# Optimization experiments

Measured on AMD Instinct MI355X. Metric: run time of the kernel, lower is better.

## Reference

```python
import jax, jax.numpy as jnp
import numpy as np

EPS = 1e-6
NUM_HEADS = 8
GAMMA = 0.999


def simple_rms_norm(x):
    # SimpleRMSNorm: x / ||x|| * sqrt(d) == x / sqrt(mean(x^2))
    return x * jax.lax.rsqrt(jnp.mean(x * x, axis=-1, keepdims=True) + EPS)


def setup_inputs() -> dict:
    key = jax.random.key(0)
    ks = jax.random.split(key, 12)
    B, N, M, E = 64, 14, 14, 512
    D1 = 2 * E              # expand_ratio * embed_dim = 1024
    RPE = 512               # rpe_embedding
    s = 0.02
    inp = {
        "x": jax.random.normal(ks[0], (B, N, M, E), jnp.float32),
        "H": N,
        "W": M,
        "Wu": jax.random.normal(ks[1], (E, D1), jnp.float32) * s,
        "bu": jnp.zeros((D1,), jnp.float32),
        "Wv": jax.random.normal(ks[2], (E, D1), jnp.float32) * s,
        "bv": jnp.zeros((D1,), jnp.float32),
        "Wo": jax.random.normal(ks[3], (D1, E), jnp.float32) * s,
        "bo": jnp.zeros((E,), jnp.float32),
        "rpe_pos_w": jax.random.normal(ks[4], (2, RPE), jnp.float32) * s,
        "rpe_pos_b": jnp.zeros((RPE,), jnp.float32),
        "rpe_w1": jax.random.normal(ks[5], (RPE, RPE), jnp.float32) * s,
        "rpe_b1": jnp.zeros((RPE,), jnp.float32),
        "rpe_w2": jax.random.normal(ks[6], (RPE, RPE), jnp.float32) * s,
        "rpe_b2": jnp.zeros((RPE,), jnp.float32),
        "rpe_w3": jax.random.normal(ks[7], (RPE, RPE), jnp.float32) * s,
        "rpe_b3": jnp.zeros((RPE,), jnp.float32),
        "rpe_out_w": jax.random.normal(ks[8], (RPE, D1), jnp.float32) * s,
        "rpe_out_b": jnp.zeros((D1,), jnp.float32),
    }
    return inp


def gtu2d_forward(x, Wu, bu, Wv, bv, Wo, bo,
                  rpe_pos_w, rpe_pos_b, rpe_w1, rpe_b1, rpe_w2, rpe_b2,
                  rpe_w3, rpe_b3, rpe_out_w, rpe_out_b):
    B, n, m, E = x.shape
    d1 = Wu.shape[1]
    hd = d1 // NUM_HEADS
    # dual gated projections
    u = jax.nn.silu(x @ Wu + bu)                      # (B, n, m, d1)
    v = jax.nn.silu(x @ Wv + bv)
    v = v.reshape(B, n, m, NUM_HEADS, hd).transpose(0, 3, 1, 2, 4)  # (B, h, n, m, d)

    # --- Tno2D: RPE MLP produces Toeplitz coefficients for relative positions ---
    ii = jnp.arange(-(n - 1), n, dtype=jnp.float32)
    jj = jnp.arange(-(m - 1), m, dtype=jnp.float32)
    pos = jnp.stack(jnp.meshgrid(ii, jj, indexing="ij"), axis=-1)  # (2n-1, 2m-1, 2)
    r = pos @ rpe_pos_w + rpe_pos_b
    for w, b in ((rpe_w1, rpe_b1), (rpe_w2, rpe_b2), (rpe_w3, rpe_b3)):
        r = jax.nn.relu(simple_rms_norm(r)) @ w + b
    r = jax.nn.relu(simple_rms_norm(r)) @ rpe_out_w + rpe_out_b  # (2n-1, 2m-1, h*d)
    a = r.reshape(2 * n - 1, 2 * m - 1, NUM_HEADS, hd).transpose(2, 0, 1, 3)
    # decay: gamma^(|i|+|j|)
    dist = jnp.abs(pos[..., 0]) + jnp.abs(pos[..., 1])  # (2n-1, 2m-1)
    a = a * (GAMMA ** dist)[None, :, :, None]

    # embed coefficients into circular kernel (h, 2n, 2m, d); index n / m are zero
    t = jnp.zeros((NUM_HEADS, 2 * n, 2 * m, hd), a.dtype)
    t = t.at[:, :n, :m].set(a[:, n - 1:, m - 1:])
    t = t.at[:, n + 1:, :m].set(a[:, :n - 1, m - 1:])
    t = t.at[:, :n, m + 1:].set(a[:, n - 1:, :m - 1])
    t = t.at[:, n + 1:, m + 1:].set(a[:, :n - 1, :m - 1])

    # 2D Toeplitz matvec via circular convolution / FFT
    xf = jnp.fft.rfft2(v, s=(2 * n, 2 * m), axes=(2, 3))
    tf = jnp.fft.rfft2(t, s=(2 * n, 2 * m), axes=(1, 2))
    y = jnp.fft.irfft2(xf * tf[None], s=(2 * n, 2 * m), axes=(2, 3))[:, :, :n, :m, :]
    y = y.transpose(0, 2, 3, 1, 4).reshape(B, n, m, d1)  # 'b h n m d -> b n m (h d)'

    return (u * y) @ Wo + bo


def reference(x, H, W, Wu, bu, Wv, bv, Wo, bo,
              rpe_pos_w, rpe_pos_b, rpe_w1, rpe_b1, rpe_w2, rpe_b2,
              rpe_w3, rpe_b3, rpe_out_w, rpe_out_b):
    # H, W are unused by Gtu2d.forward (spatial dims are carried by x)
    return gtu2d_forward(x, Wu, bu, Wv, bv, Wo, bo,
                         rpe_pos_w, rpe_pos_b, rpe_w1, rpe_b1, rpe_w2, rpe_b2,
                         rpe_w3, rpe_b3, rpe_out_w, rpe_out_b)
```

## Files before the change

### kernel.cpp

```cpp
#include <hip/hip_runtime.h>
#include <hip/hip_bf16.h>

typedef __hip_bfloat16 bf16;
typedef __attribute__((ext_vector_type(8))) short bf16x8;
typedef __attribute__((ext_vector_type(4))) float f32x4;

constexpr int NB    = 64;
constexpr int EE    = 512;
constexpr int RPOS  = 27 * 27;
constexpr int ROWS  = NB * 14 * 14;

#define RMS_EPS 1e-6f
#define GAMMA_LOG2 (-0.00144344319f)

__device__ __forceinline__ void  stf(float* p, float v) { *p = v; }
__device__ __forceinline__ void  stf(bf16* p, float v)  { *p = __float2bfloat16(v); }

__device__ __forceinline__ void gload_lds16(const bf16* g, bf16* l) {
    __builtin_amdgcn_global_load_lds(
        (const __attribute__((address_space(1))) void*)g,
        (__attribute__((address_space(3))) void*)l, 16, 0, 0);
}

#define VMCNT(n) asm volatile("s_waitcnt vmcnt(" #n ")" ::: "memory")

__global__ __launch_bounds__(256) void k_prep(const float* __restrict__ Wu,
                                              const float* __restrict__ Wv,
                                              const float* __restrict__ Wo,
                                              const float* __restrict__ w1,
                                              const float* __restrict__ w2,
                                              const float* __restrict__ w3,
                                              const float* __restrict__ wOut,
                                              const float* __restrict__ bu,
                                              const float* __restrict__ bv,
                                              const float* __restrict__ x,
                                              bf16* __restrict__ WuvT,
                                              bf16* __restrict__ WoT,
                                              bf16* __restrict__ w1T,
                                              bf16* __restrict__ w2T,
                                              bf16* __restrict__ w3T,
                                              bf16* __restrict__ wOutT,
                                              float* __restrict__ biasUv,
                                              bf16* __restrict__ xb) {
    __shared__ float t[32][33];
    const int tid = threadIdx.x;
    int b = blockIdx.x;

    const float* src = nullptr; bf16* dst = nullptr; int R = 0, C = 0, nbx = 0;
    if (b < 512)        { src = Wu;   dst = WuvT;                      R = 512;  C = 1024; nbx = 32; }
    else if (b < 1024)  { b -= 512;   src = Wv; dst = WuvT + (size_t)1024 * 512; R = 512; C = 1024; nbx = 32; }
    else if (b < 1536)  { b -= 1024;  src = Wo;   dst = WoT;           R = 1024; C = 512;  nbx = 16; }
    else if (b < 1792)  { b -= 1536;  src = w1;   dst = w1T;           R = 512;  C = 512;  nbx = 16; }
    else if (b < 2048)  { b -= 1792;  src = w2;   dst = w2T;           R = 512;  C = 512;  nbx = 16; }
    else if (b < 2304)  { b -= 2048;  src = w3;   dst = w3T;           R = 512;  C = 512;  nbx = 16; }
    else if (b < 2816)  { b -= 2304;  src = wOut; dst = wOutT;         R = 512;  C = 1024; nbx = 32; }
    else if (b < 2824) {
        int c = (b - 2816) * 256 + tid;
        if (c < 2048) biasUv[c] = (c < 1024) ? bu[c] : bv[c - 1024];
        return;
    } else {
        int i = (b - 2824) * 256 + tid;
        float4 v = *(const float4*)&x[(size_t)i * 4];
        bf16* d = &xb[(size_t)i * 4];
        d[0] = __float2bfloat16(v.x);
        d[1] = __float2bfloat16(v.y);
        d[2] = __float2bfloat16(v.z);
        d[3] = __float2bfloat16(v.w);
        return;
    }
    int bx = (b % nbx) * 32;
    int by = (b / nbx) * 32;
    int tx = tid & 31, ty = tid >> 5;
    #pragma unroll
    for (int i = 0; i < 4; ++i)
        t[ty + i * 8][tx] = src[(size_t)(by + ty + i * 8) * C + bx + tx];
    __syncthreads();
    #pragma unroll
    for (int i = 0; i < 4; ++i)
        dst[(size_t)(bx + ty + i * 8) * R + by + tx] = __float2bfloat16(t[tx][ty + i * 8]);
}

__global__ void k_rpe_pos_norm(const float* __restrict__ w, const float* __restrict__ bias,
                               bf16* __restrict__ out) {
    int p = blockIdx.x;
    float ii = (float)(p / 27 - 13);
    float jj = (float)(p % 27 - 13);
    int c0 = threadIdx.x, c1 = threadIdx.x + 256;
    float v0 = ii * w[c0] + jj * w[512 + c0] + bias[c0];
    float v1 = ii * w[c1] + jj * w[512 + c1] + bias[c1];
    float s = v0 * v0 + v1 * v1;
    #pragma unroll
    for (int off = 32; off; off >>= 1) s += __shfl_down(s, off, 64);
    __shared__ float ps[4];
    if ((threadIdx.x & 63) == 0) ps[threadIdx.x >> 6] = s;
    __syncthreads();
    float tot = ps[0] + ps[1] + ps[2] + ps[3];
    float scale = rsqrtf(tot * (1.0f / 512.0f) + RMS_EPS);
    out[(size_t)p * 512 + c0] = __float2bfloat16(fmaxf(v0 * scale, 0.0f));
    out[(size_t)p * 512 + c1] = __float2bfloat16(fmaxf(v1 * scale, 0.0f));
}

template <typename TO>
__global__ void k_rmsnorm_relu(const float* __restrict__ in, TO* __restrict__ out) {
    int r = blockIdx.x;
    const float* x = in + (size_t)r * 512;
    float v0 = x[threadIdx.x];
    float v1 = x[threadIdx.x + 256];
    float s = v0 * v0 + v1 * v1;
    #pragma unroll
    for (int off = 32; off; off >>= 1) s += __shfl_down(s, off, 64);
    __shared__ float ps[4];
    if ((threadIdx.x & 63) == 0) ps[threadIdx.x >> 6] = s;
    __syncthreads();
    float tot = ps[0] + ps[1] + ps[2] + ps[3];
    float scale = rsqrtf(tot * (1.0f / 512.0f) + RMS_EPS);
    stf(&out[(size_t)r * 512 + threadIdx.x],       fmaxf(v0 * scale, 0.0f));
    stf(&out[(size_t)r * 512 + threadIdx.x + 256], fmaxf(v1 * scale, 0.0f));
}

template <int EPI, typename TO>
__global__ __launch_bounds__(256) void k_mgemm_s(const bf16* __restrict__ A,
                                                 const bf16* __restrict__ Bt,
                                                 const float* __restrict__ bias,
                                                 TO* __restrict__ out,
                                                 int M, int N, int K) {
    __shared__ bf16 As[64 * 32];
    __shared__ bf16 Bs[64 * 32];
    const int tid = threadIdx.x;
    const int m0 = blockIdx.y * 64;
    const int n0 = blockIdx.x * 64;
    const int lane = tid & 63;
    const int w = tid >> 6;
    const int lr = lane & 15;
    const int lk = (lane >> 4) * 8;

    f32x4 acc[4] = {};
    const int row = tid >> 2;
    const int seg = (tid & 3) * 8;

    for (int k0 = 0; k0 < K; k0 += 32) {
        gload_lds16(&A[(size_t)(m0 + row) * K + k0 + seg], &As[tid * 8]);
        gload_lds16(&Bt[(size_t)(n0 + row) * K + k0 + seg], &Bs[tid * 8]);
        __syncthreads();
        bf16x8 af = *(const bf16x8*)&As[(w * 16 + lr) * 32 + lk];
        #pragma unroll
        for (int j = 0; j < 4; ++j) {
            bf16x8 bf = *(const bf16x8*)&Bs[(j * 16 + lr) * 32 + lk];
            acc[j] = __builtin_amdgcn_mfma_f32_16x16x32_bf16(af, bf, acc[j], 0, 0, 0);
        }
        __syncthreads();
    }

    const int crow = (lane >> 4) * 4;
    const int ccol = lane & 15;
    #pragma unroll
    for (int j = 0; j < 4; ++j) {
        int gc = n0 + j * 16 + ccol;
        float bb = bias[gc];
        #pragma unroll
        for (int r = 0; r < 4; ++r) {
            int gr = m0 + w * 16 + crow + r;
            if (gr < M) {
                float val = acc[j][r] + bb;
                if (EPI == 2) {
                    int i = gr / 27, jj = gr % 27;
                    val *= exp2f((float)(abs(i - 13) + abs(jj - 13)) * GAMMA_LOG2);
                }
                stf(&out[(size_t)gr * N + gc], val);
            }
        }
    }
}

template <int EPI, typename TO>
__global__ __launch_bounds__(256) void k_mgemm(const bf16* __restrict__ A, int lda,
                                               const bf16* __restrict__ Bt,
                                               const float* __restrict__ bias,
                                               TO* __restrict__ out, int ldo,
                                               int M, int N, int K) {
    __shared__ bf16 As[128 * 32];
    __shared__ bf16 Bs[128 * 32];
    const int tid = threadIdx.x;
    const int m0 = blockIdx.y * 128;
    const int n0 = blockIdx.x * 128;
    const int lane = tid & 63;
    const int w = tid >> 6;
    const int wr = (w >> 1) * 64;
    const int wc = (w & 1) * 64;
    const int lr = lane & 15;
    const int lk = (lane >> 4) * 8;

    f32x4 acc[4][4] = {};

    for (int k0 = 0; k0 < K; k0 += 32) {
        #pragma unroll
        for (int t = 0; t < 2; ++t) {
            int flat = t * 256 + tid;
            int row = flat >> 2;
            int seg = (flat & 3) * 8;
            gload_lds16(&A[(size_t)(m0 + row) * lda + k0 + seg], &As[flat * 8]);
            gload_lds16(&Bt[(size_t)(n0 + row) * K + k0 + seg], &Bs[flat * 8]);
        }
        __syncthreads();
        bf16x8 af[4], bf[4];
        #pragma unroll
        for (int i = 0; i < 4; ++i) {
            af[i] = *(const bf16x8*)&As[(wr + i * 16 + lr) * 32 + lk];
            bf[i] = *(const bf16x8*)&Bs[(wc + i * 16 + lr) * 32 + lk];
        }
        #pragma unroll
        for (int i = 0; i < 4; ++i)
            #pragma unroll
            for (int j = 0; j < 4; ++j)
                acc[i][j] = __builtin_amdgcn_mfma_f32_16x16x32_bf16(af[i], bf[j], acc[i][j], 0, 0, 0);
        __syncthreads();
    }

    const int crow = (lane >> 4) * 4;
    const int ccol = lane & 15;
    #pragma unroll
    for (int i = 0; i < 4; ++i)
        #pragma unroll
        for (int j = 0; j < 4; ++j) {
            int gc = n0 + wc + j * 16 + ccol;
            float bb = bias[gc];
            #pragma unroll
            for (int r = 0; r < 4; ++r) {
                int gr = m0 + wr + i * 16 + crow + r;
                float val = acc[i][j][r] + bb;
                if (EPI == 1) val = val / (1.0f + expf(-val));
                stf(&out[(size_t)gr * ldo + gc], val);
            }
        }
}

template <int KT, int EPI, typename TO>
__global__ __launch_bounds__(512, 2) void k_mgemm8(const bf16* __restrict__ A, int lda,
                                                   const bf16* __restrict__ Bt,
                                                   const float* __restrict__ bias,
                                                   TO* __restrict__ out, int ldo,
                                                   int nb ) {
    constexpr int K = KT * 64;
    __shared__ __align__(16) char lds[131072];

    const int tid = threadIdx.x;
    const int lane = tid & 63;
    const int wid = tid >> 6;
    const int wr = wid >> 2;
    const int wc = wid & 3;

    int wgid = blockIdx.x;
    if ((gridDim.x & 7) == 0) {
        int cpx = gridDim.x >> 3;
        wgid = (wgid & 7) * cpx + (wgid >> 3);
    }
    const int m0 = (wgid / nb) * 256;
    const int n0 = (wgid % nb) * 256;

    auto ldsA = [&](int d, int kh) -> char* { return (char*)lds + d * 32768 + kh * 16384; };
    auto ldsB = [&](int d, int kh) -> char* { return (char*)lds + 65536 + d * 32768 + kh * 16384; };

    auto stage = [&](int op, int kh, int tt) {
        char* base = op ? ldsB(tt & 1, kh) : ldsA(tt & 1, kh);
        const bf16* g = op ? Bt : A;
        const int rowbase = op ? n0 : m0;
        const int ldr = op ? K : lda;
        #pragma unroll
        for (int l = 0; l < 2; ++l) {
            int q = tid + l * 512;
            int r = q >> 2;
            int cl = (q & 3) ^ ((r ^ (r >> 2)) & 3);
            const bf16* src = g + (size_t)(rowbase + r) * ldr + tt * 64 + kh * 32 + cl * 8;
            gload_lds16(src, (bf16*)(base + q * 16));
        }
    };
    auto rdA = [&](int d, int ks, int mi) -> bf16x8 {
        int row = wr * 128 + mi * 16 + (lane & 15);
        int ch = (lane >> 4) ^ ((row ^ (row >> 2)) & 3);
        return *(const bf16x8*)(ldsA(d, ks) + row * 64 + ch * 16);
    };
    auto rdB = [&](int d, int ks, int nj) -> bf16x8 {
        int row = wc * 64 + nj * 16 + (lane & 15);
        int ch = (lane >> 4) ^ ((row ^ (row >> 2)) & 3);
        return *(const bf16x8*)(ldsB(d, ks) + row * 64 + ch * 16);
    };

    f32x4 acc[8][4] = {};
    bf16x8 aF[4], bF[4];

    stage(0, 0, 0); stage(1, 0, 0); stage(0, 1, 0); stage(1, 1, 0);
    stage(0, 0, 1); stage(1, 0, 1);
    VMCNT(8);
    __builtin_amdgcn_s_barrier();
    __builtin_amdgcn_sched_barrier(0);

    #pragma unroll
    for (int t = 0; t < KT; ++t) {
        const int d = t & 1;
        #pragma unroll
        for (int mi = 0; mi < 4; ++mi) aF[mi] = rdA(d, 0, mi);
        #pragma unroll
        for (int nj = 0; nj < 4; ++nj) bF[nj] = rdB(d, 0, nj);
        if (t + 1 < KT) stage(0, 1, t + 1);
        __builtin_amdgcn_s_barrier();
        __builtin_amdgcn_s_setprio(1);
        #pragma unroll
        for (int mi = 0; mi < 4; ++mi)
            #pragma unroll
            for (int nj = 0; nj < 4; ++nj)
                acc[mi][nj] = __builtin_amdgcn_mfma_f32_16x16x32_bf16(aF[mi], bF[nj], acc[mi][nj], 0, 0, 0);
        __builtin_amdgcn_s_setprio(0);
        __builtin_amdgcn_s_barrier();
        #pragma unroll
        for (int mi = 0; mi < 4; ++mi) aF[mi] = rdA(d, 0, mi + 4);
        if (t + 1 < KT) stage(1, 1, t + 1);
        if (t + 1 < KT) { VMCNT(8); } else { VMCNT(0); }
        __builtin_amdgcn_s_barrier();
        __builtin_amdgcn_sched_barrier(0);
        __builtin_amdgcn_s_setprio(1);
        #pragma unroll
        for (int mi = 0; mi < 4; ++mi)
            #pragma unroll
            for (int nj = 0; nj < 4; ++nj)
                acc[mi + 4][nj] = __builtin_amdgcn_mfma_f32_16x16x32_bf16(aF[mi], bF[nj], acc[mi + 4][nj], 0, 0, 0);
        __builtin_amdgcn_s_setprio(0);
        __builtin_amdgcn_s_barrier();
        #pragma unroll
        for (int mi = 0; mi < 4; ++mi) aF[mi] = rdA(d, 1, mi);
        #pragma unroll
        for (int nj = 0; nj < 4; ++nj) bF[nj] = rdB(d, 1, nj);
        if (t + 2 < KT) stage(0, 0, t + 2);
        __builtin_amdgcn_s_barrier();
        __builtin_amdgcn_s_setprio(1);
        #pragma unroll
        for (int mi = 0; mi < 4; ++mi)
            #pragma unroll
            for (int nj = 0; nj < 4; ++nj)
                acc[mi][nj] = __builtin_amdgcn_mfma_f32_16x16x32_bf16(aF[mi], bF[nj], acc[mi][nj], 0, 0, 0);
        __builtin_amdgcn_s_setprio(0);
        __builtin_amdgcn_s_barrier();
        #pragma unroll
        for (int mi = 0; mi < 4; ++mi) aF[mi] = rdA(d, 1, mi + 4);
        if (t + 2 < KT) stage(1, 0, t + 2);
        if (t + 2 < KT)      { VMCNT(8); }
        else if (t + 1 < KT) { VMCNT(4); }
        __builtin_amdgcn_s_barrier();
        __builtin_amdgcn_sched_barrier(0);
        __builtin_amdgcn_s_setprio(1);
        #pragma unroll
        for (int mi = 0; mi < 4; ++mi)
            #pragma unroll
            for (int nj = 0; nj < 4; ++nj)
                acc[mi + 4][nj] = __builtin_amdgcn_mfma_f32_16x16x32_bf16(aF[mi], bF[nj], acc[mi + 4][nj], 0, 0, 0);
        __builtin_amdgcn_s_setprio(0);
        __builtin_amdgcn_s_barrier();
    }

    const int crow = (lane >> 4) * 4;
    const int ccol = lane & 15;
    #pragma unroll
    for (int mi = 0; mi < 8; ++mi)
        #pragma unroll
        for (int nj = 0; nj < 4; ++nj) {
            int gc = n0 + wc * 64 + nj * 16 + ccol;
            float bb = bias[gc];
            #pragma unroll
            for (int r = 0; r < 4; ++r) {
                int gr = m0 + wr * 128 + mi * 16 + crow + r;
                float val = acc[mi][nj][r] + bb;
                if (EPI == 1) val = val / (1.0f + expf(-val));
                stf(&out[(size_t)gr * ldo + gc], val);
            }
        }
}

__global__ __launch_bounds__(256) void k_vt(const bf16* __restrict__ uv,
                                            bf16* __restrict__ Vt) {
    const int c0 = blockIdx.x * 64;
    const int b  = blockIdx.y;
    const int tid = threadIdx.x;
    __shared__ bf16 t[196][66];
    for (int f = tid; f < 196 * 64; f += 256) {
        int ij = f >> 6, cl = f & 63;
        t[ij][cl] = uv[((size_t)b * 196 + ij) * 2048 + 1024 + c0 + cl];
    }
    __syncthreads();
    const bf16 z = __float2bfloat16(0.0f);
    for (int f = tid; f < 64 * 224; f += 256) {
        int cl = f / 224, ij = f - cl * 224;
        Vt[((size_t)(c0 + cl) * 64 + b) * 224 + ij] = (ij < 196) ? t[ij][cl] : z;
    }
}

__global__ __launch_bounds__(256) void k_convm(const bf16* __restrict__ Ab,
                                               const bf16* __restrict__ Vt,
                                               bf16* __restrict__ Yt, int cbase) {
    __shared__ __align__(16) bf16 Ts[112 * 232];
    __shared__ bf16 As[736];
    const int mh = blockIdx.x;
    const int cl = blockIdx.y;
    const int c = cbase + cl;
    const int tid = threadIdx.x;
    const int mbase = mh * 112;

    for (int e = tid; e < 729; e += 256)
        As[e] = Ab[(size_t)e * 1024 + c];
    __syncthreads();

    const bf16 z = __float2bfloat16(0.0f);
    if (tid < 224) {
        const int i = tid / 14, j = tid - i * 14;
        const bool kvalid = tid < 196;
        int p = mbase / 14, q = 0;
        for (int r = 0; r < 112; ++r) {
            bf16 val = z;
            if (kvalid && (mbase + r) < 196)
                val = As[(p - i + 13) * 27 + (q - j + 13)];
            Ts[r * 232 + tid] = val;
            if (++q == 14) { q = 0; ++p; }
        }
    }
    __syncthreads();

    const int lane = tid & 63;
    const int w = tid >> 6;
    const int lr = lane & 15;
    const int lk = (lane >> 4) * 8;
    const bf16* Vc = Vt + (size_t)c * 64 * 224;

    bf16x8 bfr[7];
    #pragma unroll
    for (int ks = 0; ks < 7; ++ks)
        bfr[ks] = *(const bf16x8*)&Vc[(size_t)(w * 16 + lr) * 224 + ks * 32 + lk];

    f32x4 acc[7] = {};
    #pragma unroll
    for (int ks = 0; ks < 7; ++ks)
        #pragma unroll
        for (int mi = 0; mi < 7; ++mi) {
            bf16x8 a = *(const bf16x8*)&Ts[(mi * 16 + lr) * 232 + ks * 32 + lk];
            acc[mi] = __builtin_amdgcn_mfma_f32_16x16x32_bf16(a, bfr[ks], acc[mi], 0, 0, 0);
        }

    const int crow = (lane >> 4) * 4;
    const int bb = w * 16 + (lane & 15);
    #pragma unroll
    for (int mi = 0; mi < 7; ++mi) {
        int pq = mbase + mi * 16 + crow;
        #pragma unroll
        for (int r = 0; r < 4; ++r)
            if (pq + r < 196)
                Yt[((size_t)cl * 196 + pq + r) * 64 + bb] = __float2bfloat16(acc[mi][r]);
    }
}

__global__ __launch_bounds__(256) void k_gate(bf16* __restrict__ uv,
                                              const bf16* __restrict__ Yt, int cbase) {
    const int pq = blockIdx.x;
    const int ct = blockIdx.y;
    const int tid = threadIdx.x;
    __shared__ float t[64][65];
    for (int f = tid; f < 64 * 64; f += 256) {
        int cr = f >> 6, bcol = f & 63;
        t[cr][bcol] = __bfloat162float(Yt[((size_t)(ct * 64 + cr) * 196 + pq) * 64 + bcol]);
    }
    __syncthreads();
    for (int f = tid; f < 64 * 64; f += 256) {
        int br = f >> 6, cc = f & 63;
        size_t row = (size_t)br * 196 + pq;
        int cglob = cbase + ct * 64 + cc;
        float uu = __bfloat162float(uv[row * 2048 + cglob]);
        uv[row * 2048 + 1024 + cglob] = __float2bfloat16(t[cc][br] * uu);
    }
}

extern "C" void kernel_launch(void* const* d_in, const int* in_sizes, int n_in,
                              void* d_out, int out_size, void* d_ws, size_t ws_size,
                              hipStream_t stream) {
    const float* x    = (const float*)d_in[0];
    const float* Wu   = (const float*)d_in[3];
    const float* bu   = (const float*)d_in[4];
    const float* Wv   = (const float*)d_in[5];
    const float* bv   = (const float*)d_in[6];
    const float* Wo   = (const float*)d_in[7];
    const float* bo   = (const float*)d_in[8];
    const float* rpw  = (const float*)d_in[9];
    const float* rpb  = (const float*)d_in[10];
    const float* w1   = (const float*)d_in[11];
    const float* b1   = (const float*)d_in[12];
    const float* w2   = (const float*)d_in[13];
    const float* b2   = (const float*)d_in[14];
    const float* w3   = (const float*)d_in[15];
    const float* b3   = (const float*)d_in[16];
    const float* wOut = (const float*)d_in[17];
    const float* bOut = (const float*)d_in[18];

    char* ws = (char*)d_ws;
    size_t off = 0;
    auto take = [&](size_t bytes) { char* p = ws + off; off += (bytes + 255) & ~size_t(255); return p; };
    float* rA     = (float*)take((size_t)RPOS * 512 * 4);
    float* rB     = (float*)take((size_t)RPOS * 512 * 4);
    bf16*  rn     = (bf16*)take((size_t)RPOS * 512 * 2 + 40960);
    bf16*  Ab     = (bf16*)take((size_t)RPOS * 1024 * 2);
    bf16*  xb     = (bf16*)take((size_t)ROWS * EE * 2);
    bf16*  WuvT   = (bf16*)take((size_t)2048 * 512 * 2);
    bf16*  WoT    = (bf16*)take((size_t)512 * 1024 * 2);
    bf16*  w1T    = (bf16*)take((size_t)512 * 512 * 2);
    bf16*  w2T    = (bf16*)take((size_t)512 * 512 * 2);
    bf16*  w3T    = (bf16*)take((size_t)512 * 512 * 2);
    bf16*  wOutT  = (bf16*)take((size_t)1024 * 512 * 2);
    float* biasUv = (float*)take(2048 * 4);
    bf16*  uvb    = (bf16*)take((size_t)ROWS * 2048 * 2);
    bf16*  Vt     = (bf16*)take((size_t)1024 * 64 * 224 * 2);
    bf16*  Yt     = (bf16*)xb;

    k_prep<<<9096, 256, 0, stream>>>(Wu, Wv, Wo, w1, w2, w3, wOut, bu, bv, x,
                                     WuvT, WoT, w1T, w2T, w3T, wOutT, biasUv, xb);

    k_rpe_pos_norm<<<RPOS, 256, 0, stream>>>(rpw, rpb, rn);
    k_mgemm_s<0, float><<<dim3(8, 12), 256, 0, stream>>>(rn, w1T, b1, rB, RPOS, 512, 512);
    k_rmsnorm_relu<bf16><<<RPOS, 256, 0, stream>>>(rB, rn);
    k_mgemm_s<0, float><<<dim3(8, 12), 256, 0, stream>>>(rn, w2T, b2, rA, RPOS, 512, 512);
    k_rmsnorm_relu<bf16><<<RPOS, 256, 0, stream>>>(rA, rn);
    k_mgemm_s<0, float><<<dim3(8, 12), 256, 0, stream>>>(rn, w3T, b3, rB, RPOS, 512, 512);
    k_rmsnorm_relu<bf16><<<RPOS, 256, 0, stream>>>(rB, rn);
    k_mgemm_s<2, bf16><<<dim3(16, 12), 256, 0, stream>>>(rn, wOutT, bOut, Ab, RPOS, 1024, 512);

    k_mgemm8<8, 1, bf16><<<392, 512, 0, stream>>>(xb, 512, WuvT, biasUv, uvb, 2048, 8);

    k_vt<<<dim3(16, 64), 256, 0, stream>>>(uvb, Vt);

    for (int h = 0; h < 2; ++h) {
        k_convm<<<dim3(2, 512), 256, 0, stream>>>(Ab, Vt, Yt, h * 512);
        k_gate<<<dim3(196, 8), 256, 0, stream>>>(uvb, Yt, h * 512);
    }

    k_mgemm<0, float><<<dim3(4, 98), 256, 0, stream>>>(uvb + 1024, 2048, WoT, bo,
                                                       (float*)d_out, 512, ROWS, 512, 1024);
}
```

Before: 235.7 us.

## Fuse RPE RMSNorm into GEMM epilogues and merge conv/gate halves into single launches

The RMSNorm+ReLU kernels between the RPE MLP GEMMs are removed. Each GEMM now writes the ReLU'd bf16 output along with per-column-block partial sums of squares. The next GEMM rescales its accumulators by the row rsqrt factor, which works because the row scale commutes with the matmul. Separately, when the workspace has room, the two-half convm/gate loop becomes one launch each over a z-dimension, using a full-size Yt buffer. This removes three kernel launches and the fp32 intermediate traffic, and halves the conv/gate launches. The cost is an epilogue shuffle reduction and a dependence on workspace size.

Result: faster. 217.8 us (-7.6%).

```diff
diff --git a/kernel.cpp b/kernel.cpp
--- a/kernel.cpp
+++ b/kernel.cpp
@@ -100,30 +100,14 @@
     out[(size_t)p * 512 + c1] = __float2bfloat16(fmaxf(v1 * scale, 0.0f));
 }
 
-template <typename TO>
-__global__ void k_rmsnorm_relu(const float* __restrict__ in, TO* __restrict__ out) {
-    int r = blockIdx.x;
-    const float* x = in + (size_t)r * 512;
-    float v0 = x[threadIdx.x];
-    float v1 = x[threadIdx.x + 256];
-    float s = v0 * v0 + v1 * v1;
-    #pragma unroll
-    for (int off = 32; off; off >>= 1) s += __shfl_down(s, off, 64);
-    __shared__ float ps[4];
-    if ((threadIdx.x & 63) == 0) ps[threadIdx.x >> 6] = s;
-    __syncthreads();
-    float tot = ps[0] + ps[1] + ps[2] + ps[3];
-    float scale = rsqrtf(tot * (1.0f / 512.0f) + RMS_EPS);
-    stf(&out[(size_t)r * 512 + threadIdx.x],       fmaxf(v0 * scale, 0.0f));
-    stf(&out[(size_t)r * 512 + threadIdx.x + 256], fmaxf(v1 * scale, 0.0f));
-}
-
-template <int EPI, typename TO>
-__global__ __launch_bounds__(256) void k_mgemm_s(const bf16* __restrict__ A,
-                                                 const bf16* __restrict__ Bt,
-                                                 const float* __restrict__ bias,
-                                                 TO* __restrict__ out,
-                                                 int M, int N, int K) {
+template <int SCALE_IN, int EPI>
+__global__ __launch_bounds__(256) void k_rpe_gemm(const bf16* __restrict__ A,
+                                                  const bf16* __restrict__ Bt,
+                                                  const float* __restrict__ bias,
+                                                  const float* __restrict__ pIn,
+                                                  float* __restrict__ pOut,
+                                                  bf16* __restrict__ out,
+                                                  int M, int N, int K) {
     __shared__ bf16 As[64 * 32];
     __shared__ bf16 Bs[64 * 32];
     const int tid = threadIdx.x;
@@ -153,6 +137,20 @@
 
     const int crow = (lane >> 4) * 4;
     const int ccol = lane & 15;
+    float sc[4];
+    #pragma unroll
+    for (int r = 0; r < 4; ++r) {
+        sc[r] = 1.0f;
+        if (SCALE_IN) {
+            int gr = m0 + w * 16 + crow + r;
+            if (gr < M) {
+                const float* pp = &pIn[(size_t)gr * 8];
+                float s8 = pp[0] + pp[1] + pp[2] + pp[3] + pp[4] + pp[5] + pp[6] + pp[7];
+                sc[r] = rsqrtf(s8 * (1.0f / 512.0f) + RMS_EPS);
+            }
+        }
+    }
+    float rowsq[4] = {0.f, 0.f, 0.f, 0.f};
     #pragma unroll
     for (int j = 0; j < 4; ++j) {
         int gc = n0 + j * 16 + ccol;
@@ -160,13 +158,30 @@
         #pragma unroll
         for (int r = 0; r < 4; ++r) {
             int gr = m0 + w * 16 + crow + r;
-            if (gr < M) {
-                float val = acc[j][r] + bb;
-                if (EPI == 2) {
+            float val = acc[j][r] * sc[r] + bb;
+            if (EPI == 0) {
+                rowsq[r] += val * val;
+                if (gr < M) out[(size_t)gr * N + gc] = __float2bfloat16(fmaxf(val, 0.0f));
+            } else {
+                if (gr < M) {
                     int i = gr / 27, jj = gr % 27;
-                    val *= exp2f((float)(abs(i - 13) + abs(jj - 13)) * GAMMA_LOG2);
+                    float decay = exp2f((float)(abs(i - 13) + abs(jj - 13)) * GAMMA_LOG2);
+                    out[(size_t)gr * N + gc] = __float2bfloat16(val * decay);
                 }
-                stf(&out[(size_t)gr * N + gc], val);
+            }
+        }
+    }
+    if (EPI == 0) {
+        #pragma unroll
+        for (int r = 0; r < 4; ++r) {
+            #pragma unroll
+            for (int m = 1; m < 16; m <<= 1) rowsq[r] += __shfl_xor(rowsq[r], m, 64);
+        }
+        if ((lane & 15) == 0) {
+            #pragma unroll
+            for (int r = 0; r < 4; ++r) {
+                int gr = m0 + w * 16 + crow + r;
+                if (gr < M) pOut[(size_t)gr * 8 + blockIdx.x] = rowsq[r];
             }
         }
     }
@@ -392,6 +407,7 @@
     }
 }
 
+template <int ZBIG>
 __global__ __launch_bounds__(256) void k_convm(const bf16* __restrict__ Ab,
                                                const bf16* __restrict__ Vt,
                                                bf16* __restrict__ Yt, int cbase) {
@@ -399,7 +415,9 @@
     __shared__ bf16 As[736];
     const int mh = blockIdx.x;
     const int cl = blockIdx.y;
-    const int c = cbase + cl;
+    const int cb = ZBIG ? (int)blockIdx.z * 512 : cbase;
+    const int c = cb + cl;
+    const int ytc = ZBIG ? c : cl;
     const int tid = threadIdx.x;
     const int mbase = mh * 112;
 
@@ -450,25 +468,28 @@
         #pragma unroll
         for (int r = 0; r < 4; ++r)
             if (pq + r < 196)
-                Yt[((size_t)cl * 196 + pq + r) * 64 + bb] = __float2bfloat16(acc[mi][r]);
-    }
-}
-
+                Yt[((size_t)ytc * 196 + pq + r) * 64 + bb] = __float2bfloat16(acc[mi][r]);
+    }
+}
+
+template <int ZBIG>
 __global__ __launch_bounds__(256) void k_gate(bf16* __restrict__ uv,
                                               const bf16* __restrict__ Yt, int cbase) {
     const int pq = blockIdx.x;
     const int ct = blockIdx.y;
+    const int cb = ZBIG ? (int)blockIdx.z * 512 : cbase;
+    const int ytb = ZBIG ? cb : 0;
     const int tid = threadIdx.x;
     __shared__ float t[64][65];
     for (int f = tid; f < 64 * 64; f += 256) {
         int cr = f >> 6, bcol = f & 63;
-        t[cr][bcol] = __bfloat162float(Yt[((size_t)(ct * 64 + cr) * 196 + pq) * 64 + bcol]);
+        t[cr][bcol] = __bfloat162float(Yt[((size_t)(ytb + ct * 64 + cr) * 196 + pq) * 64 + bcol]);
     }
     __syncthreads();
     for (int f = tid; f < 64 * 64; f += 256) {
         int br = f >> 6, cc = f & 63;
         size_t row = (size_t)br * 196 + pq;
-        int cglob = cbase + ct * 64 + cc;
+        int cglob = cb + ct * 64 + cc;
         float uu = __bfloat162float(uv[row * 2048 + cglob]);
         uv[row * 2048 + 1024 + cglob] = __float2bfloat16(t[cc][br] * uu);
     }
@@ -498,9 +519,11 @@
     char* ws = (char*)d_ws;
     size_t off = 0;
     auto take = [&](size_t bytes) { char* p = ws + off; off += (bytes + 255) & ~size_t(255); return p; };
-    float* rA     = (float*)take((size_t)RPOS * 512 * 4);
-    float* rB     = (float*)take((size_t)RPOS * 512 * 4);
-    bf16*  rn     = (bf16*)take((size_t)RPOS * 512 * 2 + 40960);
+    bf16*  rnA    = (bf16*)take((size_t)768 * 512 * 2);
+    bf16*  rnB    = (bf16*)take((size_t)768 * 512 * 2);
+    float* p1     = (float*)take((size_t)768 * 8 * 4);
+    float* p2     = (float*)take((size_t)768 * 8 * 4);
+    float* p3     = (float*)take((size_t)768 * 8 * 4);
     bf16*  Ab     = (bf16*)take((size_t)RPOS * 1024 * 2);
     bf16*  xb     = (bf16*)take((size_t)ROWS * EE * 2);
     bf16*  WuvT   = (bf16*)take((size_t)2048 * 512 * 2);
@@ -512,27 +535,33 @@
     float* biasUv = (float*)take(2048 * 4);
     bf16*  uvb    = (bf16*)take((size_t)ROWS * 2048 * 2);
     bf16*  Vt     = (bf16*)take((size_t)1024 * 64 * 224 * 2);
-    bf16*  Yt     = (bf16*)xb;
+
+    const size_t ytFullBytes = (size_t)1024 * 196 * 64 * 2;
+    bool bigYt = (off + ytFullBytes) <= ws_size;
+    bf16* YtFull = bigYt ? (bf16*)(ws + off) : nullptr;
+    bf16* YtHalf = (bf16*)xb;
 
     k_prep<<<9096, 256, 0, stream>>>(Wu, Wv, Wo, w1, w2, w3, wOut, bu, bv, x,
                                      WuvT, WoT, w1T, w2T, w3T, wOutT, biasUv, xb);
 
-    k_rpe_pos_norm<<<RPOS, 256, 0, stream>>>(rpw, rpb, rn);
-    k_mgemm_s<0, float><<<dim3(8, 12), 256, 0, stream>>>(rn, w1T, b1, rB, RPOS, 512, 512);
-    k_rmsnorm_relu<bf16><<<RPOS, 256, 0, stream>>>(rB, rn);
-    k_mgemm_s<0, float><<<dim3(8, 12), 256, 0, stream>>>(rn, w2T, b2, rA, RPOS, 512, 512);
-    k_rmsnorm_relu<bf16><<<RPOS, 256, 0, stream>>>(rA, rn);
-    k_mgemm_s<0, float><<<dim3(8, 12), 256, 0, stream>>>(rn, w3T, b3, rB, RPOS, 512, 512);
-    k_rmsnorm_relu<bf16><<<RPOS, 256, 0, stream>>>(rB, rn);
-    k_mgemm_s<2, bf16><<<dim3(16, 12), 256, 0, stream>>>(rn, wOutT, bOut, Ab, RPOS, 1024, 512);
+    k_rpe_pos_norm<<<RPOS, 256, 0, stream>>>(rpw, rpb, rnA);
+    k_rpe_gemm<0, 0><<<dim3(8, 12), 256, 0, stream>>>(rnA, w1T, b1, nullptr, p1, rnB, RPOS, 512, 512);
+    k_rpe_gemm<1, 0><<<dim3(8, 12), 256, 0, stream>>>(rnB, w2T, b2, p1, p2, rnA, RPOS, 512, 512);
+    k_rpe_gemm<1, 0><<<dim3(8, 12), 256, 0, stream>>>(rnA, w3T, b3, p2, p3, rnB, RPOS, 512, 512);
+    k_rpe_gemm<1, 2><<<dim3(16, 12), 256, 0, stream>>>(rnB, wOutT, bOut, p3, nullptr, Ab, RPOS, 1024, 512);
 
     k_mgemm8<8, 1, bf16><<<392, 512, 0, stream>>>(xb, 512, WuvT, biasUv, uvb, 2048, 8);
 
     k_vt<<<dim3(16, 64), 256, 0, stream>>>(uvb, Vt);
 
-    for (int h = 0; h < 2; ++h) {
-        k_convm<<<dim3(2, 512), 256, 0, stream>>>(Ab, Vt, Yt, h * 512);
-        k_gate<<<dim3(196, 8), 256, 0, stream>>>(uvb, Yt, h * 512);
+    if (bigYt) {
+        k_convm<1><<<dim3(2, 512, 2), 256, 0, stream>>>(Ab, Vt, YtFull, 0);
+        k_gate<1><<<dim3(196, 8, 2), 256, 0, stream>>>(uvb, YtFull, 0);
+    } else {
+        for (int h = 0; h < 2; ++h) {
+            k_convm<0><<<dim3(2, 512), 256, 0, stream>>>(Ab, Vt, YtHalf, h * 512);
+            k_gate<0><<<dim3(196, 8), 256, 0, stream>>>(uvb, YtHalf, h * 512);
+        }
     }
 
     k_mgemm<0, float><<<dim3(4, 98), 256, 0, stream>>>(uvb + 1024, 2048, WoT, bo,
```
